# Kernel optimization log

Measured on AMD Instinct MI355X. Metric: run time of the kernel, lower is better.

## Reference

```python
import jax, jax.numpy as jnp
import numpy as np

OUT_FEATURES = 4096
IN_FEATURES = 4096
GROUP_SIZE = 128
NUM_GROUPS = OUT_FEATURES // GROUP_SIZE  # groups along output-channel axis (axis=0)


def _unpack_int8_to_int4(packed, num_elements):
    # Each int8 byte holds two signed int4 values: low nibble first, then high nibble.
    p = packed.astype(jnp.int8)
    low = jnp.right_shift(jnp.left_shift(p, 4), 4)   # sign-extended low nibble, in [-8, 7]
    high = jnp.right_shift(p, 4)                      # arithmetic shift -> sign-extended high nibble
    vals = jnp.stack([low, high], axis=-1).reshape(-1)
    return vals[:num_elements]


def _dequantize_weight(packed_weight, scales, zero_points):
    int4 = _unpack_int8_to_int4(packed_weight, OUT_FEATURES * IN_FEATURES)
    w = int4.astype(jnp.float32).reshape(NUM_GROUPS, GROUP_SIZE, IN_FEATURES)
    # per-group (over output channels): (q - zp) * scale
    w = (w - zero_points[:, None, None]) * scales[:, None, None]
    return w.reshape(OUT_FEATURES, IN_FEATURES)


def setup_inputs() -> dict:
    key = jax.random.key(0)
    k_x, k_w, k_s, k_zp, k_b = jax.random.split(key, 5)
    x = jax.random.normal(k_x, (8192, IN_FEATURES), dtype=jnp.float32)
    # packed int4 weights stored as signed bytes
    packed_weight = jax.random.randint(k_w, (OUT_FEATURES * IN_FEATURES // 2,), 0, 256, dtype=jnp.int32) - 128
    scales = jax.random.uniform(k_s, (NUM_GROUPS,), dtype=jnp.float32) * 0.02 + 0.001
    zero_points = jax.random.normal(k_zp, (NUM_GROUPS,), dtype=jnp.float32) * 0.5
    bias = jax.random.normal(k_b, (OUT_FEATURES,), dtype=jnp.float32)
    return {"x": x, "packed_weight": packed_weight, "scales": scales,
            "zero_points": zero_points, "bias": bias}


def reference(x, packed_weight, scales, zero_points, bias):
    weight = _dequantize_weight(packed_weight, scales, zero_points)  # [out, in]
    return jnp.einsum('bi,oi->bo', x, weight) + bias
```

## Files before the change

kernel.cpp:

```cpp
#include <hip/hip_runtime.h>
#include <cstdint>
#include <cstddef>

#define M_DIM 8192
#define N_DIM 4096
#define K_DIM 4096
#define CHUNK_M 4096

typedef __attribute__((ext_vector_type(8))) short bf16x8;
typedef __attribute__((ext_vector_type(4))) float floatx4;

__device__ __forceinline__ ushort f2bf_rne(float f) {
    union { float f; uint32_t u; } a;
    a.f = f;
    uint32_t u = a.u;
    uint32_t r = (u + 0x7fffu + ((u >> 16) & 1u)) >> 16;
    return (ushort)r;
}

__device__ __forceinline__ uint32_t pk_bf_trunc(float f0, float f1) {
    return __builtin_amdgcn_perm(__float_as_uint(f1), __float_as_uint(f0),
                                 0x07060302u);
}

__global__ void dequant_w_kernel(const int4* __restrict__ pw,
                                 const float* __restrict__ scales,
                                 const float* __restrict__ zps,
                                 uint4* __restrict__ wb, int np4) {
    int p4 = blockIdx.x * blockDim.x + threadIdx.x;
    if (p4 >= np4) return;
    int p = p4 * 4;
    int g = p >> 18;
    float s = scales[g];
    float b = -zps[g] * s;
    int4 v = pw[p4];
    int vv[4] = { v.x, v.y, v.z, v.w };
    ushort o[8];
#pragma unroll
    for (int j = 0; j < 4; ++j) {
        int lo = ((int)((uint32_t)vv[j] << 28)) >> 28;
        int hi = ((int)((uint32_t)vv[j] << 24)) >> 28;
        o[2 * j]     = f2bf_rne(fmaf((float)lo, s, b));
        o[2 * j + 1] = f2bf_rne(fmaf((float)hi, s, b));
    }
    uint4 st;
    st.x = (uint32_t)o[0] | ((uint32_t)o[1] << 16);
    st.y = (uint32_t)o[2] | ((uint32_t)o[3] << 16);
    st.z = (uint32_t)o[4] | ((uint32_t)o[5] << 16);
    st.w = (uint32_t)o[6] | ((uint32_t)o[7] << 16);
    wb[p4] = st;
}

__global__ void convert_x_kernel(const float4* __restrict__ x4,
                                 ushort4* __restrict__ out4, int n4) {
    int i = blockIdx.x * blockDim.x + threadIdx.x;
    if (i >= n4) return;
    float4 v = x4[i];
    ushort4 o;
    o.x = f2bf_rne(v.x);
    o.y = f2bf_rne(v.y);
    o.z = f2bf_rne(v.z);
    o.w = f2bf_rne(v.w);
    out4[i] = o;
}

#define TBM 256
#define TBN 256
#define TBK 32
#define NT  (K_DIM / TBK)
#define A_E 8192
#define SLOT_E 16384

__global__ __launch_bounds__(512, 2)
void gemm_bf16_256(const ushort* __restrict__ A,
                   const ushort* __restrict__ B,
                   const float* __restrict__ bias,
                   float* __restrict__ C) {
    __shared__ ushort lds[4 * SLOT_E];

    const int tid  = threadIdx.x;
    const int lane = tid & 63;
    const int wave = tid >> 6;
    const int wm   = wave >> 2;
    const int wn   = wave & 3;

    const int nwg = gridDim.x;
    const int cpx = nwg >> 3;
    const int bid = blockIdx.x;
    const int swz = (bid & 7) * cpx + (bid >> 3);
    const int bn  = swz & (N_DIM / TBN - 1);
    const int bm  = swz / (N_DIM / TBN);

    const ushort* Ab = A + (size_t)(bm * TBM) * K_DIM;
    const ushort* Bb = B + (size_t)(bn * TBN) * K_DIM;

    const int srow = tid >> 2;
    const int scol = (((tid & 3) ^ ((tid >> 3) & 3)) * 8);
    const ushort* gA0 = Ab + (size_t)srow * K_DIM + scol;
    const ushort* gA1 = gA0 + (size_t)128 * K_DIM;
    const ushort* gB0 = Bb + (size_t)srow * K_DIM + scol;
    const ushort* gB1 = gB0 + (size_t)128 * K_DIM;
    const int wdst = wave * 512;

    const int frow = lane & 15;
    const int fcol = (((lane >> 4) ^ ((frow >> 1) & 3)) * 8);
    const int aoff = (wm * 128 + frow) * TBK + fcol;
    const int boff = A_E + (wn * 64 + frow) * TBK + fcol;

    floatx4 acc[8][4] = {};

#define STAGE_A(tt)                                                           \
    {                                                                          \
        const int k0s = ((tt) & (NT - 1)) * TBK;                               \
        ushort* d = lds + ((tt) & 3) * SLOT_E + wdst;                          \
        __builtin_amdgcn_global_load_lds(                                      \
            (const __attribute__((address_space(1))) void*)(gA0 + k0s),        \
            (__attribute__((address_space(3))) void*)d, 16, 0, 0);             \
        __builtin_amdgcn_global_load_lds(                                      \
            (const __attribute__((address_space(1))) void*)(gA1 + k0s),        \
            (__attribute__((address_space(3))) void*)(d + 4096), 16, 0, 0);    \
    }
#define STAGE_B(tt)                                                           \
    {                                                                          \
        const int k0s = ((tt) & (NT - 1)) * TBK;                               \
        ushort* d = lds + ((tt) & 3) * SLOT_E + A_E + wdst;                    \
        __builtin_amdgcn_global_load_lds(                                      \
            (const __attribute__((address_space(1))) void*)(gB0 + k0s),        \
            (__attribute__((address_space(3))) void*)d, 16, 0, 0);             \
        __builtin_amdgcn_global_load_lds(                                      \
            (const __attribute__((address_space(1))) void*)(gB1 + k0s),        \
            (__attribute__((address_space(3))) void*)(d + 4096), 16, 0, 0);    \
    }

#define BODY(T, afc, bfc, afn, bfn)                                           \
    {                                                                          \
        const ushort* bnxt = lds + (((T) + 1) & 3) * SLOT_E;                   \
                                             \
        _Pragma("unroll")                                                      \
        for (int i = 0; i < 4; ++i)                                            \
            afn[i] = *(const bf16x8*)(bnxt + aoff + i * 512);                  \
        STAGE_A((T) + 3)                                                       \
        __builtin_amdgcn_sched_barrier(0);                                     \
        __builtin_amdgcn_s_setprio(1);                                         \
        _Pragma("unroll")                                                      \
        for (int i = 0; i < 2; ++i)                                            \
            _Pragma("unroll")                                                  \
            for (int j = 0; j < 4; ++j)                                        \
                acc[i][j] = __builtin_amdgcn_mfma_f32_16x16x32_bf16(           \
                    afc[i], bfc[j], acc[i][j], 0, 0, 0);                       \
        __builtin_amdgcn_s_setprio(0);                                         \
        __builtin_amdgcn_sched_barrier(0);                                     \
                                             \
        _Pragma("unroll")                                                      \
        for (int j = 0; j < 4; ++j)                                            \
            bfn[j] = *(const bf16x8*)(bnxt + boff + j * 512);                  \
        STAGE_B((T) + 3)                                                       \
        __builtin_amdgcn_sched_barrier(0);                                     \
        __builtin_amdgcn_s_setprio(1);                                         \
        _Pragma("unroll")                                                      \
        for (int i = 2; i < 4; ++i)                                            \
            _Pragma("unroll")                                                  \
            for (int j = 0; j < 4; ++j)                                        \
                acc[i][j] = __builtin_amdgcn_mfma_f32_16x16x32_bf16(           \
                    afc[i], bfc[j], acc[i][j], 0, 0, 0);                       \
        __builtin_amdgcn_s_setprio(0);                                         \
        __builtin_amdgcn_sched_barrier(0);                                     \
                                                            \
        _Pragma("unroll")                                                      \
        for (int i = 4; i < 8; ++i)                                            \
            afn[i] = *(const bf16x8*)(bnxt + aoff + i * 512);                  \
        __builtin_amdgcn_sched_barrier(0);                                     \
        __builtin_amdgcn_s_setprio(1);                                         \
        _Pragma("unroll")                                                      \
        for (int i = 4; i < 8; ++i)                                            \
            _Pragma("unroll")                                                  \
            for (int j = 0; j < 4; ++j)                                        \
                acc[i][j] = __builtin_amdgcn_mfma_f32_16x16x32_bf16(           \
                    afc[i], bfc[j], acc[i][j], 0, 0, 0);                       \
        __builtin_amdgcn_s_setprio(0);                                         \
                        \
        asm volatile("s_waitcnt vmcnt(4)" ::: "memory");                       \
        __builtin_amdgcn_s_barrier();                                          \
        __builtin_amdgcn_sched_barrier(0);                                     \
    }

    STAGE_A(0) STAGE_B(0)
    STAGE_A(1) STAGE_B(1)
    STAGE_A(2) STAGE_B(2)
    asm volatile("s_waitcnt vmcnt(4)" ::: "memory");
    __builtin_amdgcn_s_barrier();
    __builtin_amdgcn_sched_barrier(0);

    bf16x8 af0[8], bf0[4], af1[8], bf1[4];
#pragma unroll
    for (int j = 0; j < 4; ++j)
        bf0[j] = *(const bf16x8*)(lds + boff + j * 512);
#pragma unroll
    for (int i = 0; i < 8; ++i)
        af0[i] = *(const bf16x8*)(lds + aoff + i * 512);

    for (int t = 0; t < NT; t += 2) {
        BODY(t,     af0, bf0, af1, bf1)
        BODY(t + 1, af1, bf1, af0, bf0)
    }
#undef BODY
#undef STAGE_A
#undef STAGE_B

    const int crow0 = bm * TBM + wm * 128;
    const int ccol0 = bn * TBN + wn * 64;
    const int rl = lane >> 4;
    const int cl = lane & 15;
#pragma unroll
    for (int j = 0; j < 4; ++j) {
        const int col = ccol0 + j * 16 + cl;
        const float bv = bias[col];
#pragma unroll
        for (int i = 0; i < 8; ++i) {
            const int row = crow0 + i * 16 + rl * 4;
            float* cp = C + (size_t)row * N_DIM + col;
#pragma unroll
            for (int r = 0; r < 4; ++r)
                cp[(size_t)r * N_DIM] = acc[i][j][r] + bv;
        }
    }
}

#define BM 128
#define BN 128
#define BK 32

__global__ void gemm_fused_kernel(const float* __restrict__ X,
                                  const ushort* __restrict__ B,
                                  const float* __restrict__ bias,
                                  float* __restrict__ C) {
    __shared__ ushort As[BM * BK];
    __shared__ ushort Bs[BN * BK];

    const int tid  = threadIdx.x;
    const int lane = tid & 63;
    const int wave = tid >> 6;
    const int wm   = wave >> 1;
    const int wn   = wave & 1;
    const int bm   = blockIdx.y;
    const int bn   = blockIdx.x;

    const int ar = tid >> 2;
    const int ac = (tid & 3) * 8;
    const float* xp0 = X + (size_t)(bm * BM + ar) * K_DIM + ac;
    const float* xp1 = xp0 + (size_t)64 * K_DIM;
    ushort* as0 = As + ar * BK + ac;
    ushort* as1 = as0 + 64 * BK;

    const int scol = (lane & 3) * 8;
    const ushort* Bb = B + (size_t)(bn * BN) * K_DIM;

    floatx4 acc[4][4] = {};

    for (int k0 = 0; k0 < K_DIM; k0 += BK) {
        float4 a0 = *(const float4*)(xp0 + k0);
        float4 a1 = *(const float4*)(xp0 + k0 + 4);
        float4 b0 = *(const float4*)(xp1 + k0);
        float4 b1 = *(const float4*)(xp1 + k0 + 4);
#pragma unroll
        for (int q = 0; q < 2; ++q) {
            const int chunk = wave * 2 + q;
            const int r = chunk * 16 + (lane >> 2);
            const ushort* gb = Bb + (size_t)r * K_DIM + k0 + scol;
            __builtin_amdgcn_global_load_lds(
                (const __attribute__((address_space(1))) void*)gb,
                (__attribute__((address_space(3))) void*)(Bs + chunk * 512),
                16, 0, 0);
        }
        uint4 w0, w1;
        w0.x = pk_bf_trunc(a0.x, a0.y);
        w0.y = pk_bf_trunc(a0.z, a0.w);
        w0.z = pk_bf_trunc(a1.x, a1.y);
        w0.w = pk_bf_trunc(a1.z, a1.w);
        w1.x = pk_bf_trunc(b0.x, b0.y);
        w1.y = pk_bf_trunc(b0.z, b0.w);
        w1.z = pk_bf_trunc(b1.x, b1.y);
        w1.w = pk_bf_trunc(b1.z, b1.w);
        *(uint4*)as0 = w0;
        *(uint4*)as1 = w1;

        __syncthreads();

        bf16x8 af[4], bfr[4];
        const int frow = lane & 15;
        const int fcol = (lane >> 4) * 8;
#pragma unroll
        for (int i = 0; i < 4; ++i) {
            af[i]  = *(const bf16x8*)(As + (wm * 64 + i * 16 + frow) * BK + fcol);
            bfr[i] = *(const bf16x8*)(Bs + (wn * 64 + i * 16 + frow) * BK + fcol);
        }
#pragma unroll
        for (int i = 0; i < 4; ++i)
#pragma unroll
            for (int j = 0; j < 4; ++j)
                acc[i][j] = __builtin_amdgcn_mfma_f32_16x16x32_bf16(
                    af[i], bfr[j], acc[i][j], 0, 0, 0);
        __syncthreads();
    }

    const int crow0 = bm * BM + wm * 64;
    const int ccol0 = bn * BN + wn * 64;
    const int rl = lane >> 4;
    const int cl = lane & 15;
#pragma unroll
    for (int j = 0; j < 4; ++j) {
        const int col = ccol0 + j * 16 + cl;
        const float bv = bias[col];
#pragma unroll
        for (int i = 0; i < 4; ++i) {
            const int row = crow0 + i * 16 + rl * 4;
            float* cp = C + (size_t)row * N_DIM + col;
#pragma unroll
            for (int r = 0; r < 4; ++r)
                cp[(size_t)r * N_DIM] = acc[i][j][r] + bv;
        }
    }
}

extern "C" void kernel_launch(void* const* d_in, const int* in_sizes, int n_in,
                              void* d_out, int out_size, void* d_ws, size_t ws_size,
                              hipStream_t stream) {
    const float* x      = (const float*)d_in[0];
    const int*   pw     = (const int*)d_in[1];
    const float* scales = (const float*)d_in[2];
    const float* zps    = (const float*)d_in[3];
    const float* bias   = (const float*)d_in[4];
    float* out = (float*)d_out;

    ushort* wb = (ushort*)d_ws;

    {
        int np4 = (N_DIM * K_DIM / 2) / 4;
        dequant_w_kernel<<<np4 / 256, 256, 0, stream>>>(
            (const int4*)pw, scales, zps, (uint4*)wb, np4);
    }

    const size_t need_full  = ((size_t)N_DIM * K_DIM + (size_t)M_DIM * K_DIM) * 2;
    const size_t need_chunk = ((size_t)N_DIM * K_DIM + (size_t)CHUNK_M * K_DIM) * 2;

    if (ws_size >= need_full) {
        ushort* xb = wb + (size_t)N_DIM * K_DIM;
        int n4 = (M_DIM * K_DIM) / 4;
        convert_x_kernel<<<n4 / 256, 256, 0, stream>>>(
            (const float4*)x, (ushort4*)xb, n4);
        int nblk = (M_DIM / TBM) * (N_DIM / TBN);
        gemm_bf16_256<<<nblk, 512, 0, stream>>>(xb, wb, bias, out);
    } else if (ws_size >= need_chunk) {
        ushort* xb = wb + (size_t)N_DIM * K_DIM;
        for (int c = 0; c < M_DIM / CHUNK_M; ++c) {
            const float* xc = x + (size_t)c * CHUNK_M * K_DIM;
            float* oc = out + (size_t)c * CHUNK_M * N_DIM;
            int n4 = (CHUNK_M * K_DIM) / 4;
            convert_x_kernel<<<n4 / 256, 256, 0, stream>>>(
                (const float4*)xc, (ushort4*)xb, n4);
            int nblk = (CHUNK_M / TBM) * (N_DIM / TBN);
            gemm_bf16_256<<<nblk, 512, 0, stream>>>(xb, wb, bias, oc);
        }
    } else {
        dim3 grid(N_DIM / BN, M_DIM / BM);
        gemm_fused_kernel<<<grid, 256, 0, stream>>>(x, wb, bias, out);
    }
}
```

Measured before the change: 463.9 us.

## Load B fragments directly from global memory into registers, bypassing LDS

The B tile is no longer staged through LDS with async global-to-LDS copies. Each wave now reads its own B fragments straight from global memory into registers, one k-step ahead, and the LDS slots shrink to hold only A. The aim is to cut LDS traffic and the LDS footprint for B. In exchange, the two waves that share a column block both fetch the same B data, and B gets only one iteration of prefetch to hide global latency instead of the earlier three-stage pipeline.

```diff
diff --git a/kernel.cpp b/kernel.cpp
--- a/kernel.cpp
+++ b/kernel.cpp
@@ -68,8 +68,7 @@
 #define TBN 256
 #define TBK 32
 #define NT  (K_DIM / TBK)
-#define A_E 8192
-#define SLOT_E 16384
+#define SLOT_E 8192
 
 __global__ __launch_bounds__(512, 2)
 void gemm_bf16_256(const ushort* __restrict__ A,
@@ -92,20 +91,19 @@
     const int bm  = swz / (N_DIM / TBN);
 
     const ushort* Ab = A + (size_t)(bm * TBM) * K_DIM;
-    const ushort* Bb = B + (size_t)(bn * TBN) * K_DIM;
 
     const int srow = tid >> 2;
     const int scol = (((tid & 3) ^ ((tid >> 3) & 3)) * 8);
     const ushort* gA0 = Ab + (size_t)srow * K_DIM + scol;
     const ushort* gA1 = gA0 + (size_t)128 * K_DIM;
-    const ushort* gB0 = Bb + (size_t)srow * K_DIM + scol;
-    const ushort* gB1 = gB0 + (size_t)128 * K_DIM;
     const int wdst = wave * 512;
 
     const int frow = lane & 15;
-    const int fcol = (((lane >> 4) ^ ((frow >> 1) & 3)) * 8);
-    const int aoff = (wm * 128 + frow) * TBK + fcol;
-    const int boff = A_E + (wn * 64 + frow) * TBK + fcol;
+    const int fcolA = (((lane >> 4) ^ ((frow >> 1) & 3)) * 8);
+    const int aoff = (wm * 128 + frow) * TBK + fcolA;
+
+    const ushort* gBf = B + (size_t)(bn * TBN + wn * 64 + frow) * K_DIM +
+                        (lane >> 4) * 8;
 
     floatx4 acc[8][4] = {};
 
@@ -120,20 +118,18 @@
             (const __attribute__((address_space(1))) void*)(gA1 + k0s),        \
             (__attribute__((address_space(3))) void*)(d + 4096), 16, 0, 0);    \
     }
-#define STAGE_B(tt)                                                           \
+
+#define LOAD_B(tt, bfr)                                                       \
     {                                                                          \
-        const int k0s = ((tt) & (NT - 1)) * TBK;                               \
-        ushort* d = lds + ((tt) & 3) * SLOT_E + A_E + wdst;                    \
-        __builtin_amdgcn_global_load_lds(                                      \
-            (const __attribute__((address_space(1))) void*)(gB0 + k0s),        \
-            (__attribute__((address_space(3))) void*)d, 16, 0, 0);             \
-        __builtin_amdgcn_global_load_lds(                                      \
-            (const __attribute__((address_space(1))) void*)(gB1 + k0s),        \
-            (__attribute__((address_space(3))) void*)(d + 4096), 16, 0, 0);    \
+        const size_t bk = (size_t)((tt) & (NT - 1)) * TBK;                     \
+        _Pragma("unroll")                                                      \
+        for (int j = 0; j < 4; ++j)                                            \
+            bfr[j] = *(const bf16x8*)(gBf + (size_t)j * 16 * K_DIM + bk);      \
     }
 
 #define BODY(T, afc, bfc, afn, bfn)                                           \
     {                                                                          \
+        LOAD_B((T) + 1, bfn)                                                   \
         const ushort* bnxt = lds + (((T) + 1) & 3) * SLOT_E;                   \
                                              \
         _Pragma("unroll")                                                      \
@@ -150,11 +146,10 @@
                     afc[i], bfc[j], acc[i][j], 0, 0, 0);                       \
         __builtin_amdgcn_s_setprio(0);                                         \
         __builtin_amdgcn_sched_barrier(0);                                     \
-                                             \
-        _Pragma("unroll")                                                      \
-        for (int j = 0; j < 4; ++j)                                            \
-            bfn[j] = *(const bf16x8*)(bnxt + boff + j * 512);                  \
-        STAGE_B((T) + 3)                                                       \
+                                                            \
+        _Pragma("unroll")                                                      \
+        for (int i = 4; i < 8; ++i)                                            \
+            afn[i] = *(const bf16x8*)(bnxt + aoff + i * 512);                  \
         __builtin_amdgcn_sched_barrier(0);                                     \
         __builtin_amdgcn_s_setprio(1);                                         \
         _Pragma("unroll")                                                      \
@@ -165,11 +160,7 @@
                     afc[i], bfc[j], acc[i][j], 0, 0, 0);                       \
         __builtin_amdgcn_s_setprio(0);                                         \
         __builtin_amdgcn_sched_barrier(0);                                     \
-                                                            \
-        _Pragma("unroll")                                                      \
-        for (int i = 4; i < 8; ++i)                                            \
-            afn[i] = *(const bf16x8*)(bnxt + aoff + i * 512);                  \
-        __builtin_amdgcn_sched_barrier(0);                                     \
+                                                    \
         __builtin_amdgcn_s_setprio(1);                                         \
         _Pragma("unroll")                                                      \
         for (int i = 4; i < 8; ++i)                                            \
@@ -178,23 +169,19 @@
                 acc[i][j] = __builtin_amdgcn_mfma_f32_16x16x32_bf16(           \
                     afc[i], bfc[j], acc[i][j], 0, 0, 0);                       \
         __builtin_amdgcn_s_setprio(0);                                         \
-                        \
-        asm volatile("s_waitcnt vmcnt(4)" ::: "memory");                       \
+              \
+        asm volatile("s_waitcnt vmcnt(2)" ::: "memory");                       \
         __builtin_amdgcn_s_barrier();                                          \
         __builtin_amdgcn_sched_barrier(0);                                     \
     }
 
-    STAGE_A(0) STAGE_B(0)
-    STAGE_A(1) STAGE_B(1)
-    STAGE_A(2) STAGE_B(2)
-    asm volatile("s_waitcnt vmcnt(4)" ::: "memory");
+    bf16x8 af0[8], bf0[4], af1[8], bf1[4];
+    LOAD_B(0, bf0)
+    STAGE_A(0) STAGE_A(1) STAGE_A(2)
+    asm volatile("s_waitcnt vmcnt(2)" ::: "memory");
     __builtin_amdgcn_s_barrier();
     __builtin_amdgcn_sched_barrier(0);
 
-    bf16x8 af0[8], bf0[4], af1[8], bf1[4];
-#pragma unroll
-    for (int j = 0; j < 4; ++j)
-        bf0[j] = *(const bf16x8*)(lds + boff + j * 512);
 #pragma unroll
     for (int i = 0; i < 8; ++i)
         af0[i] = *(const bf16x8*)(lds + aoff + i * 512);
@@ -204,8 +191,8 @@
         BODY(t + 1, af1, bf1, af0, bf0)
     }
 #undef BODY
+#undef LOAD_B
 #undef STAGE_A
-#undef STAGE_B
 
     const int crow0 = bm * TBM + wm * 128;
     const int ccol0 = bn * TBN + wn * 64;
```

Measured after the change: 613.8 us. 1.32x slower.
